# Kernel optimization log

Hardware: AMD Instinct MI355X
Metric: run time of the kernel (lower is better)

The kernel has to match this reference:

```python
import jax, jax.numpy as jnp
import numpy as np

LN_EPS = 1e-5
WKV_EPS = 1e-8


def _layernorm(x, g, b):
    mu = jnp.mean(x, axis=-1, keepdims=True)
    var = jnp.mean((x - mu) ** 2, axis=-1, keepdims=True)
    return (x - mu) * jax.lax.rsqrt(var + LN_EPS) * g + b


def setup_inputs() -> dict:
    key = jax.random.key(0)
    ks = jax.random.split(key, 16)
    B, S, D, F = 4, 2048, 1024, 4096
    xavier_d = float(np.sqrt(6.0 / (D + D)))
    xavier_df = float(np.sqrt(6.0 / (D + F)))
    u = lambda k, sh, s: jax.random.uniform(k, sh, jnp.float32, -s, s)
    return {
        "x": jax.random.normal(ks[0], (B, S, D), jnp.float32),
        "ln1_g": jnp.ones((D,), jnp.float32),
        "ln1_b": jnp.zeros((D,), jnp.float32),
        "ln2_g": jnp.ones((D,), jnp.float32),
        "ln2_b": jnp.zeros((D,), jnp.float32),
        "Wr": u(ks[1], (D, D), xavier_d),
        "Ww": u(ks[2], (D, D), xavier_d),
        "Wk": u(ks[3], (D, D), xavier_d),
        "Wv": u(ks[4], (D, D), xavier_d),
        "Wo": u(ks[5], (D, D), xavier_d),
        "time_decay": jax.random.uniform(ks[6], (D,), jnp.float32, -1.0, 0.0),
        "time_first": jax.random.uniform(ks[7], (D,), jnp.float32, -1.0, 1.0),
        "Wkey": u(ks[8], (F, D), xavier_df),
        "Wval": u(ks[9], (D, F), xavier_df),
        "Wrec": u(ks[10], (D, D), xavier_d),
    }


def _time_mix(xn, Wr, Ww, Wk, Wv, Wo, time_decay):
    # xn: [B,S,D]
    r = jax.nn.sigmoid(jnp.einsum('bsd,ed->bse', xn, Wr))
    w = -jnp.exp(jnp.einsum('bsd,ed->bse', xn, Ww))
    k = jnp.einsum('bsd,ed->bse', xn, Wk)
    v = jnp.einsum('bsd,ed->bse', xn, Wv)
    ewk = jnp.exp(w + k)  # [B,S,D]
    decay = jnp.exp(time_decay)  # [D]

    def step(carry, inp):
        num, den = carry
        e, vt = inp
        num = decay * num + e * vt
        den = decay * den + e
        wkv = num / (den + WKV_EPS)
        return (num, den), wkv

    B, S, D = xn.shape
    init = (jnp.zeros((B, D), xn.dtype), jnp.zeros((B, D), xn.dtype))
    (num_f, den_f), wkv = jax.lax.scan(
        step, init, (jnp.swapaxes(ewk, 0, 1), jnp.swapaxes(v, 0, 1)))
    wkv = jnp.swapaxes(wkv, 0, 1)  # [B,S,D]
    out = jnp.einsum('bsd,ed->bse', r * wkv, Wo)
    final_state = jnp.stack([num_f, den_f], axis=1)  # [B,2,D]
    return out, final_state


def _channel_mix(xn, Wkey, Wval, Wrec):
    k = jnp.einsum('bsd,fd->bsf', xn, Wkey)
    k = jnp.square(jax.nn.relu(k))
    v = jnp.einsum('bsf,df->bsd', k, Wval)
    r = jax.nn.sigmoid(jnp.einsum('bsd,ed->bse', xn, Wrec))
    return r * v


def reference(x, ln1_g, ln1_b, ln2_g, ln2_b, Wr, Ww, Wk, Wv, Wo,
              time_decay, time_first, Wkey, Wval, Wrec):
    tm, new_state = _time_mix(_layernorm(x, ln1_g, ln1_b),
                              Wr, Ww, Wk, Wv, Wo, time_decay)
    x = x + tm
    x = x + _channel_mix(_layernorm(x, ln2_g, ln2_b), Wkey, Wval, Wrec)
    return x, new_state
```

## Files before the change

### kernel.cpp

```cpp
#include <hip/hip_runtime.h>
#include <hip/hip_bf16.h>
#include <cstdint>
#include <cstddef>

using bf16 = __hip_bfloat16;
typedef __bf16 bf16x8 __attribute__((ext_vector_type(8)));
typedef float floatx4 __attribute__((ext_vector_type(4)));

#define LN_EPS 1e-5f
#define WKV_EPS 1e-8f

static constexpr int Bdim = 4, S = 2048, D = 1024, F = 4096;
static constexpr int M = Bdim * S;
static constexpr int NCH = 64, CH = S / NCH;
static constexpr uint32_t FP32_MAGIC = 0x3F800000u;

__device__ __forceinline__ bool is_fp32(const uint32_t* flagp) {
    return *flagp == FP32_MAGIC;
}
__device__ __forceinline__ float loadf(const void* p, size_t i, bool f32) {
    return f32 ? ((const float*)p)[i] : __bfloat162float(((const bf16*)p)[i]);
}

__device__ __forceinline__ void gload_lds16(const void* g, void* l) {
    __builtin_amdgcn_global_load_lds(
        (__attribute__((address_space(1))) void*)(g),
        (__attribute__((address_space(3))) void*)(l), 16, 0, 0);
}

__device__ __forceinline__ bf16x8 sigmoid8(bf16x8 v) {
    bf16x8 o;
    #pragma unroll
    for (int e = 0; e < 8; e++) {
        const float f = (float)v[e];
        o[e] = (__bf16)(1.0f / (1.0f + __expf(-f)));
    }
    return o;
}
__device__ __forceinline__ bf16x8 relusq8(bf16x8 v) {
    bf16x8 o;
    #pragma unroll
    for (int e = 0; e < 8; e++) {
        const float f = fmaxf((float)v[e], 0.0f);
        o[e] = (__bf16)(f * f);
    }
    return o;
}

struct WcvtArgs {
    const void* src[7];
    bf16*       dst[7];
};
__global__ __launch_bounds__(256)
void wcvt(WcvtArgs a, const uint32_t* __restrict__ flagp)
{
    const bool f32 = is_fp32(flagp);
    const int64_t idx = (int64_t)blockIdx.x * 256 + threadIdx.x;
    int seg, off;
    if (idx < (int64_t)6 * 1048576) {
        seg = (int)(idx >> 20); off = (int)(idx & 1048575);
    } else {
        seg = 6; off = (int)(idx - (int64_t)6 * 1048576);
    }
    a.dst[seg][off] = __float2bfloat16(loadf(a.src[seg], off, f32));
}
__global__ __launch_bounds__(256)
void wcvt2(const void* __restrict__ src, bf16* __restrict__ dst,
           const uint32_t* __restrict__ flagp)
{
    const bool f32 = is_fp32(flagp);
    const int idx = blockIdx.x * 256 + threadIdx.x;
    dst[idx] = __float2bfloat16(loadf(src, idx, f32));
}

enum { EPI_QKVW = 1, EPI_KR = 2 };

struct QkvwOut { bf16 *r, *g, *k, *v; };

template<int EPI>
__global__ __launch_bounds__(256)
void gemm_bt(const bf16* __restrict__ A, const bf16* __restrict__ Bw,
             void* __restrict__ outp, void* __restrict__ aux2,
             QkvwOut qo, int K, int N, const uint32_t* __restrict__ flagp)
{
    __shared__ __align__(16) bf16 smem[8192];
    bf16* sA = smem;
    bf16* sB = smem + 4096;
    const int t = threadIdx.x;
    const int tn = blockIdx.x, tm = blockIdx.y;
    const int lane = t & 63, wv = t >> 6;
    const int wm = wv & 1, wn = wv >> 1;
    const int ml = lane & 15, quad = lane >> 4;

    const size_t rowB = (size_t)K * 2;
    const char* gA = (const char*)(A) + (size_t)(tm * 128) * rowB;
    const char* gB = (const char*)(Bw) + (size_t)(tn * 128) * rowB;
    const int r  = t >> 2;
    const int cb = (((t & 3) ^ ((t >> 3) & 3)) << 4);
    const char* a0 = gA + (size_t)r * rowB + cb;
    const char* a1 = gA + (size_t)(r + 64) * rowB + cb;
    const char* b0 = gB + (size_t)r * rowB + cb;
    const char* b1 = gB + (size_t)(r + 64) * rowB + cb;
    char* lA0 = (char*)sA + t * 16;
    char* lA1 = (char*)sA + t * 16 + 4096;
    char* lB0 = (char*)sB + t * 16;
    char* lB1 = (char*)sB + t * 16 + 4096;

    floatx4 acc[4][4] = {};
    const int rq = ((quad ^ ((ml >> 1) & 3)) << 4);

    for (int k0 = 0; k0 < K; k0 += 32) {
        gload_lds16(a0, lA0);
        gload_lds16(a1, lA1);
        gload_lds16(b0, lB0);
        gload_lds16(b1, lB1);
        a0 += 64; a1 += 64; b0 += 64; b1 += 64;
        __syncthreads();
        bf16x8 af[4], bfr[4];
        #pragma unroll
        for (int i = 0; i < 4; i++) {
            af[i]  = *(const bf16x8*)((const char*)sA + (wm * 64 + i * 16 + ml) * 64 + rq);
            bfr[i] = *(const bf16x8*)((const char*)sB + (wn * 64 + i * 16 + ml) * 64 + rq);
        }
        #pragma unroll
        for (int i = 0; i < 4; i++)
            #pragma unroll
            for (int j = 0; j < 4; j++)
                acc[i][j] = __builtin_amdgcn_mfma_f32_16x16x32_bf16(af[i], bfr[j], acc[i][j], 0, 0, 0);
        __syncthreads();
    }

    constexpr int PS = 132;
    const int lwr = wm * 16 + quad * 4;
    const int lwc = wn * 64 + ml;
    const int rr = t >> 3;
    const int rc = (t & 7) * 16;
    #pragma unroll
    for (int i = 0; i < 4; i++) {
        __syncthreads();
        #pragma unroll
        for (int j = 0; j < 4; j++)
            #pragma unroll
            for (int rg = 0; rg < 4; rg++)
                smem[(lwr + rg) * PS + lwc + j * 16] = __float2bfloat16(acc[i][j][rg]);
        __syncthreads();
        const int gr = tm * 128 + ((rr < 16) ? (i * 16 + rr) : (64 + i * 16 + rr - 16));
        bf16x8 v0 = *(const bf16x8*)&smem[rr * PS + rc];
        bf16x8 v1 = *(const bf16x8*)&smem[rr * PS + rc + 8];
        const int gcol = tn * 128 + rc;
        if constexpr (EPI == EPI_QKVW) {
            const int seg = gcol >> 10;
            bf16* dst = (seg == 0) ? qo.r : (seg == 1) ? qo.g : (seg == 2) ? qo.k : qo.v;
            const size_t i2 = (size_t)gr * 1024 + (gcol & 1023);
            if (seg == 0) { v0 = sigmoid8(v0); v1 = sigmoid8(v1); }
            *(bf16x8*)&dst[i2]     = v0;
            *(bf16x8*)&dst[i2 + 8] = v1;
        } else {
            if (tn < 8) {
                const size_t i2 = (size_t)gr * 1024 + gcol;
                *(bf16x8*)&((bf16*)aux2)[i2]     = sigmoid8(v0);
                *(bf16x8*)&((bf16*)aux2)[i2 + 8] = sigmoid8(v1);
            } else {
                const size_t i2 = (size_t)gr * 4096 + (gcol - 1024);
                *(bf16x8*)&((bf16*)outp)[i2]     = relusq8(v0);
                *(bf16x8*)&((bf16*)outp)[i2 + 8] = relusq8(v1);
            }
        }
    }
}

enum { EPI64_ADDX = 0, EPI64_FINAL = 1 };

template<int EPI>
__global__ __launch_bounds__(256)
void gemm_n64(const bf16* __restrict__ A, const bf16* __restrict__ Bw,
              void* __restrict__ outp, const void* __restrict__ aux1,
              const void* __restrict__ aux2, int K, int N,
              const uint32_t* __restrict__ flagp)
{
    __shared__ __align__(16) bf16 smem[6144];
    bf16* sA = smem;
    bf16* sB = smem + 4096;
    const int t = threadIdx.x;
    const int tn = blockIdx.x, tm = blockIdx.y;
    const int lane = t & 63, wv = t >> 6;
    const int wm = wv & 1, wn = wv >> 1;
    const int ml = lane & 15, quad = lane >> 4;

    const size_t rowB = (size_t)K * 2;
    const char* gA = (const char*)(A) + (size_t)(tm * 128) * rowB;
    const char* gB = (const char*)(Bw) + (size_t)(tn * 64) * rowB;
    const int r  = t >> 2;
    const int cb = (((t & 3) ^ ((t >> 3) & 3)) << 4);
    const char* a0 = gA + (size_t)r * rowB + cb;
    const char* a1 = gA + (size_t)(r + 64) * rowB + cb;
    const char* b0 = gB + (size_t)r * rowB + cb;
    char* lA0 = (char*)sA + t * 16;
    char* lA1 = (char*)sA + t * 16 + 4096;
    char* lB0 = (char*)sB + t * 16;

    floatx4 acc[4][2] = {};
    const int rq = ((quad ^ ((ml >> 1) & 3)) << 4);

    for (int k0 = 0; k0 < K; k0 += 32) {
        gload_lds16(a0, lA0);
        gload_lds16(a1, lA1);
        gload_lds16(b0, lB0);
        a0 += 64; a1 += 64; b0 += 64;
        __syncthreads();
        bf16x8 af[4], bfr[2];
        #pragma unroll
        for (int i = 0; i < 4; i++)
            af[i]  = *(const bf16x8*)((const char*)sA + (wm * 64 + i * 16 + ml) * 64 + rq);
        #pragma unroll
        for (int j = 0; j < 2; j++)
            bfr[j] = *(const bf16x8*)((const char*)sB + (wn * 32 + j * 16 + ml) * 64 + rq);
        #pragma unroll
        for (int i = 0; i < 4; i++)
            #pragma unroll
            for (int j = 0; j < 2; j++)
                acc[i][j] = __builtin_amdgcn_mfma_f32_16x16x32_bf16(af[i], bfr[j], acc[i][j], 0, 0, 0);
        __syncthreads();
    }

    const bool f32 = is_fp32(flagp);
    constexpr int PS = 68;
    const int lwr = wm * 16 + quad * 4;
    const int lwc = wn * 32 + ml;
    const int rr = t >> 3;
    const int rc = (t & 7) * 8;
    #pragma unroll
    for (int i = 0; i < 4; i++) {
        __syncthreads();
        #pragma unroll
        for (int j = 0; j < 2; j++)
            #pragma unroll
            for (int rg = 0; rg < 4; rg++)
                smem[(lwr + rg) * PS + lwc + j * 16] = __float2bfloat16(acc[i][j][rg]);
        __syncthreads();
        const int gr = tm * 128 + ((rr < 16) ? (i * 16 + rr) : (64 + i * 16 + rr - 16));
        bf16x8 v = *(const bf16x8*)&smem[rr * PS + rc];
        const size_t idx = (size_t)gr * N + tn * 64 + rc;
        if constexpr (EPI == EPI64_ADDX) {
            bf16x8 o;
            if (f32) {
                const float4* xp = (const float4*)((const float*)aux1 + idx);
                const float4 xa = xp[0], xb = xp[1];
                o[0] = (__bf16)((float)v[0] + xa.x); o[1] = (__bf16)((float)v[1] + xa.y);
                o[2] = (__bf16)((float)v[2] + xa.z); o[3] = (__bf16)((float)v[3] + xa.w);
                o[4] = (__bf16)((float)v[4] + xb.x); o[5] = (__bf16)((float)v[5] + xb.y);
                o[6] = (__bf16)((float)v[6] + xb.z); o[7] = (__bf16)((float)v[7] + xb.w);
            } else {
                const bf16x8 xv = *(const bf16x8*)((const bf16*)aux1 + idx);
                #pragma unroll
                for (int e = 0; e < 8; e++) o[e] = (__bf16)((float)v[e] + (float)xv[e]);
            }
            *(bf16x8*)((bf16*)outp + idx) = o;
        } else {
            const bf16x8 x2v = *(const bf16x8*)((const bf16*)aux1 + idx);
            const bf16x8 rv  = *(const bf16x8*)((const bf16*)aux2 + idx);
            float ov[8];
            #pragma unroll
            for (int e = 0; e < 8; e++)
                ov[e] = (float)x2v[e] + (float)rv[e] * (float)v[e];
            if (f32) {
                float4 f0 = { ov[0], ov[1], ov[2], ov[3] };
                float4 f1 = { ov[4], ov[5], ov[6], ov[7] };
                float4* op = (float4*)((float*)outp + idx);
                op[0] = f0; op[1] = f1;
            } else {
                bf16x8 o;
                #pragma unroll
                for (int e = 0; e < 8; e++) o[e] = (__bf16)ov[e];
                *(bf16x8*)((bf16*)outp + idx) = o;
            }
        }
    }
}

template<bool IN_WS>
__global__ __launch_bounds__(256)
void ln_kernel(const void* __restrict__ x, const void* __restrict__ g,
               const void* __restrict__ b, bf16* __restrict__ out,
               const uint32_t* __restrict__ flagp)
{
    const bool f32 = is_fp32(flagp);
    const int row = blockIdx.x;
    const int t = threadIdx.x;
    const size_t base = (size_t)row * D;
    float v[4];
    #pragma unroll
    for (int i = 0; i < 4; i++) {
        const size_t c = base + t + 256 * i;
        if constexpr (IN_WS) v[i] = __bfloat162float(((const bf16*)x)[c]);
        else                 v[i] = loadf(x, c, f32);
    }
    float s = v[0] + v[1] + v[2] + v[3];
    float q = v[0]*v[0] + v[1]*v[1] + v[2]*v[2] + v[3]*v[3];
    #pragma unroll
    for (int off = 32; off > 0; off >>= 1) {
        s += __shfl_down(s, off);
        q += __shfl_down(q, off);
    }
    __shared__ float rs_[4], rq_[4];
    const int wv = t >> 6, lane = t & 63;
    if (lane == 0) { rs_[wv] = s; rq_[wv] = q; }
    __syncthreads();
    const float St = rs_[0] + rs_[1] + rs_[2] + rs_[3];
    const float Qt = rq_[0] + rq_[1] + rq_[2] + rq_[3];
    const float mean = St * (1.0f / 1024.0f);
    const float var  = Qt * (1.0f / 1024.0f) - mean * mean;
    const float rstd = rsqrtf(var + LN_EPS);
    #pragma unroll
    for (int i = 0; i < 4; i++) {
        const int c = t + 256 * i;
        const float gv = loadf(g, c, f32);
        const float bv = loadf(b, c, f32);
        out[base + c] = __float2bfloat16((v[i] - mean) * rstd * gv + bv);
    }
}

__global__ __launch_bounds__(256)
void scan_a(const bf16* __restrict__ gw, const bf16* __restrict__ kk,
            const bf16* __restrict__ vbuf, const void* __restrict__ td,
            float* __restrict__ numc, float* __restrict__ denc,
            const uint32_t* __restrict__ flagp)
{
    const bool f32 = is_fp32(flagp);
    const int idx = blockIdx.x * 256 + threadIdx.x;
    const int d = idx & (D - 1);
    const int c = (idx >> 10) & (NCH - 1);
    const int b = idx >> 16;
    const float a = __expf(loadf(td, d, f32));
    size_t p = ((size_t)b * S + (size_t)c * CH) * D + d;
    float num = 0.f, den = 0.f;
    for (int ts = 0; ts < CH; ts++) {
        const float g  = __bfloat162float(gw[p]);
        const float kv = __bfloat162float(kk[p]);
        const float e  = __expf(kv - __expf(g));
        const float vv = __bfloat162float(vbuf[p]);
        num = fmaf(a, num, e * vv);
        den = fmaf(a, den, e);
        p += D;
    }
    const size_t slot = ((size_t)b * NCH + c) * D + d;
    numc[slot] = num;
    denc[slot] = den;
}

__global__ __launch_bounds__(256)
void scan_b(float* __restrict__ numc, float* __restrict__ denc,
            const void* __restrict__ td, void* __restrict__ d_out,
            const uint32_t* __restrict__ flagp)
{
    const bool f32 = is_fp32(flagp);
    const int idx = blockIdx.x * 256 + threadIdx.x;
    const int d = idx & (D - 1);
    const int b = idx >> 10;
    const float aL = __expf(loadf(td, d, f32) * (float)CH);
    float cn = 0.f, cd = 0.f;
    for (int c = 0; c < NCH; c++) {
        const size_t slot = ((size_t)b * NCH + c) * D + d;
        const float ln = numc[slot], ld = denc[slot];
        numc[slot] = cn;
        denc[slot] = cd;
        cn = fmaf(aL, cn, ln);
        cd = fmaf(aL, cd, ld);
    }
    const size_t i0 = (size_t)b * 2 * D + d;
    const size_t i1 = i0 + D;
    const size_t off = (size_t)M * D;
    if (f32) {
        ((float*)d_out)[off + i0] = cn;
        ((float*)d_out)[off + i1] = cd;
    } else {
        ((bf16*)d_out)[off + i0] = __float2bfloat16(cn);
        ((bf16*)d_out)[off + i1] = __float2bfloat16(cd);
    }
}

__global__ __launch_bounds__(256)
void scan_c(const bf16* __restrict__ gw, const bf16* __restrict__ kk,
            const bf16* __restrict__ vbuf, bf16* __restrict__ rbuf,
            const float* __restrict__ numc, const float* __restrict__ denc,
            const void* __restrict__ td, const uint32_t* __restrict__ flagp)
{
    const bool f32 = is_fp32(flagp);
    const int idx = blockIdx.x * 256 + threadIdx.x;
    const int d = idx & (D - 1);
    const int c = (idx >> 10) & (NCH - 1);
    const int b = idx >> 16;
    const float a = __expf(loadf(td, d, f32));
    const size_t slot = ((size_t)b * NCH + c) * D + d;
    float num = numc[slot], den = denc[slot];
    size_t p = ((size_t)b * S + (size_t)c * CH) * D + d;
    for (int ts = 0; ts < CH; ts++) {
        const float g  = __bfloat162float(gw[p]);
        const float kv = __bfloat162float(kk[p]);
        const float e  = __expf(kv - __expf(g));
        const float vv = __bfloat162float(vbuf[p]);
        num = fmaf(a, num, e * vv);
        den = fmaf(a, den, e);
        const float wkv = num / (den + WKV_EPS);
        const float r = __bfloat162float(rbuf[p]);
        rbuf[p] = __float2bfloat16(r * wkv);
        p += D;
    }
}

extern "C" void kernel_launch(void* const* d_in, const int* in_sizes, int n_in,
                              void* d_out, int out_size, void* d_ws, size_t ws_size,
                              hipStream_t stream)
{
    const void* x     = d_in[0];
    const void* ln1_g = d_in[1];
    const void* ln1_b = d_in[2];
    const void* ln2_g = d_in[3];
    const void* ln2_b = d_in[4];
    const void* Wr    = d_in[5];
    const void* Ww    = d_in[6];
    const void* Wk    = d_in[7];
    const void* Wv    = d_in[8];
    const void* Wo    = d_in[9];
    const void* td    = d_in[10];
    const void* Wkey  = d_in[12];
    const void* Wval  = d_in[13];
    const void* Wrec  = d_in[14];
    const uint32_t* flagp = (const uint32_t*)ln1_g;

    #define MB(x) ((size_t)(x) << 20)
    char* ws = (char*)d_ws;
    bf16*  xnb    = (bf16*) (ws + MB(0));
    bf16*  wWval2 = (bf16*) (ws + MB(0));
    bf16*  gw     = (bf16*) (ws + MB(16));
    bf16*  kk     = (bf16*) (ws + MB(32));
    bf16*  vbuf   = (bf16*) (ws + MB(48));
    bf16*  wqkvw  = (bf16*) (ws + MB(64));
    bf16*  wWo    = (bf16*) (ws + MB(72));
    float* numc   = (float*)(ws + MB(74));
    float* denc   = (float*)(ws + MB(75));
    bf16*  kbuf   = (bf16*) (ws + MB(16));
    bf16*  rbuf   = (bf16*) (ws + MB(80));
    bf16*  x2     = (bf16*) (ws + MB(96));
    bf16*  wrk    = (bf16*) (ws + MB(112));
    #undef MB

    dim3 blk(256);
    dim3 gQ(F / 128, M / 128);
    dim3 gKR(5120 / 128, M / 128);
    dim3 g64(D / 64, M / 128);

    WcvtArgs wa;
    wa.src[0] = Wr;   wa.dst[0] = wqkvw;
    wa.src[1] = Ww;   wa.dst[1] = wqkvw + (size_t)1 * 1048576;
    wa.src[2] = Wk;   wa.dst[2] = wqkvw + (size_t)2 * 1048576;
    wa.src[3] = Wv;   wa.dst[3] = wqkvw + (size_t)3 * 1048576;
    wa.src[4] = Wo;   wa.dst[4] = wWo;
    wa.src[5] = Wrec; wa.dst[5] = wrk;
    wa.src[6] = Wkey; wa.dst[6] = wrk + (size_t)1048576;

    QkvwOut qo = { rbuf, gw, kk, vbuf };
    QkvwOut q0 = { nullptr, nullptr, nullptr, nullptr };

    wcvt<<<(10 * 1048576) / 256, blk, 0, stream>>>(wa, flagp);
    ln_kernel<false><<<M, blk, 0, stream>>>(x, ln1_g, ln1_b, xnb, flagp);
    gemm_bt<EPI_QKVW><<<gQ, blk, 0, stream>>>(xnb, wqkvw, nullptr, nullptr, qo, D, 4096, flagp);
    scan_a<<<(Bdim * NCH * D) / 256, blk, 0, stream>>>(gw, kk, vbuf, td, numc, denc, flagp);
    scan_b<<<(Bdim * D) / 256,       blk, 0, stream>>>(numc, denc, td, d_out, flagp);
    scan_c<<<(Bdim * NCH * D) / 256, blk, 0, stream>>>(gw, kk, vbuf, rbuf, numc, denc, td, flagp);
    gemm_n64<EPI64_ADDX><<<g64, blk, 0, stream>>>(rbuf, wWo, x2, x, nullptr, D, D, flagp);
    ln_kernel<true><<<M, blk, 0, stream>>>(x2, ln2_g, ln2_b, xnb, flagp);
    gemm_bt<EPI_KR><<<gKR, blk, 0, stream>>>(xnb, wrk, kbuf, rbuf, q0, D, 5120, flagp);
    wcvt2<<<(4 * 1048576) / 256, blk, 0, stream>>>(Wval, wWval2, flagp);
    gemm_n64<EPI64_FINAL><<<g64, blk, 0, stream>>>(kbuf, wWval2, d_out, x2, rbuf, F, D, flagp);
}
```

Baseline: 589.8 us.

## Unify GEMMs into one 512-thread 128x128 kernel with 64-wide K steps

Replaces the two GEMM kernels with a single 512-thread (8-wave) kernel using 128x128 output tiles and a K step of 64 in place of 32. It uses a new XOR swizzle over 128-byte LDS rows and handles all four epilogues. The aim is to halve the barrier count per K, give the N=1024 GEMMs larger tiles for better data reuse, and raise the number of waves per CU. In exchange it uses more LDS per block, and the N=1024 GEMMs now launch half as many blocks, which may hurt load balance.

```diff
diff --git a/kernel.cpp b/kernel.cpp
--- a/kernel.cpp
+++ b/kernel.cpp
@@ -73,19 +73,19 @@
     dst[idx] = __float2bfloat16(loadf(src, idx, f32));
 }
 
-enum { EPI_QKVW = 1, EPI_KR = 2 };
+enum { EPI_QKVW = 1, EPI_KR = 2, EPI_ADDX = 3, EPI_FINAL = 4 };
 
 struct QkvwOut { bf16 *r, *g, *k, *v; };
 
 template<int EPI>
-__global__ __launch_bounds__(256)
+__global__ __launch_bounds__(512, 4)
 void gemm_bt(const bf16* __restrict__ A, const bf16* __restrict__ Bw,
-             void* __restrict__ outp, void* __restrict__ aux2,
-             QkvwOut qo, int K, int N, const uint32_t* __restrict__ flagp)
-{
-    __shared__ __align__(16) bf16 smem[8192];
-    bf16* sA = smem;
-    bf16* sB = smem + 4096;
+             void* __restrict__ outp, const void* __restrict__ aux1,
+             void* __restrict__ aux2, QkvwOut qo, int K, int N,
+             const uint32_t* __restrict__ flagp)
+{
+    __shared__ __align__(16) bf16 smem[16384];
+    char* smb = (char*)smem;
     const int t = threadIdx.x;
     const int tn = blockIdx.x, tm = blockIdx.y;
     const int lane = t & 63, wv = t >> 6;
@@ -93,142 +93,56 @@
     const int ml = lane & 15, quad = lane >> 4;
 
     const size_t rowB = (size_t)K * 2;
-    const char* gA = (const char*)(A) + (size_t)(tm * 128) * rowB;
+    const int r0 = t >> 3;
+    const int q0 = (t & 7) ^ (r0 & 7);
+    const char* gA = (const char*)(A)  + (size_t)(tm * 128) * rowB;
     const char* gB = (const char*)(Bw) + (size_t)(tn * 128) * rowB;
-    const int r  = t >> 2;
-    const int cb = (((t & 3) ^ ((t >> 3) & 3)) << 4);
-    const char* a0 = gA + (size_t)r * rowB + cb;
-    const char* a1 = gA + (size_t)(r + 64) * rowB + cb;
-    const char* b0 = gB + (size_t)r * rowB + cb;
-    const char* b1 = gB + (size_t)(r + 64) * rowB + cb;
-    char* lA0 = (char*)sA + t * 16;
-    char* lA1 = (char*)sA + t * 16 + 4096;
-    char* lB0 = (char*)sB + t * 16;
-    char* lB1 = (char*)sB + t * 16 + 4096;
-
-    floatx4 acc[4][4] = {};
-    const int rq = ((quad ^ ((ml >> 1) & 3)) << 4);
-
-    for (int k0 = 0; k0 < K; k0 += 32) {
+    const char* a0 = gA + (size_t)r0 * rowB + q0 * 16;
+    const char* a1 = a0 + 64 * rowB;
+    const char* b0 = gB + (size_t)r0 * rowB + q0 * 16;
+    const char* b1 = b0 + 64 * rowB;
+    char* lA0 = smb + t * 16;
+    char* lA1 = smb + t * 16 + 8192;
+    char* lB0 = smb + t * 16 + 16384;
+    char* lB1 = smb + t * 16 + 24576;
+
+    floatx4 acc[4][2] = {};
+    const int m7 = ml & 7;
+    const int rq0 = ((quad)     ^ m7) * 16;
+    const int rq1 = ((4 + quad) ^ m7) * 16;
+
+    for (int k0 = 0; k0 < K; k0 += 64) {
         gload_lds16(a0, lA0);
         gload_lds16(a1, lA1);
         gload_lds16(b0, lB0);
         gload_lds16(b1, lB1);
-        a0 += 64; a1 += 64; b0 += 64; b1 += 64;
-        __syncthreads();
-        bf16x8 af[4], bfr[4];
-        #pragma unroll
-        for (int i = 0; i < 4; i++) {
-            af[i]  = *(const bf16x8*)((const char*)sA + (wm * 64 + i * 16 + ml) * 64 + rq);
-            bfr[i] = *(const bf16x8*)((const char*)sB + (wn * 64 + i * 16 + ml) * 64 + rq);
-        }
-        #pragma unroll
-        for (int i = 0; i < 4; i++)
-            #pragma unroll
-            for (int j = 0; j < 4; j++)
-                acc[i][j] = __builtin_amdgcn_mfma_f32_16x16x32_bf16(af[i], bfr[j], acc[i][j], 0, 0, 0);
-        __syncthreads();
-    }
-
-    constexpr int PS = 132;
-    const int lwr = wm * 16 + quad * 4;
-    const int lwc = wn * 64 + ml;
-    const int rr = t >> 3;
-    const int rc = (t & 7) * 16;
-    #pragma unroll
-    for (int i = 0; i < 4; i++) {
+        a0 += 128; a1 += 128; b0 += 128; b1 += 128;
         __syncthreads();
         #pragma unroll
-        for (int j = 0; j < 4; j++)
+        for (int kh = 0; kh < 2; kh++) {
+            const int rq = kh ? rq1 : rq0;
+            bf16x8 af[4], bfr[2];
             #pragma unroll
-            for (int rg = 0; rg < 4; rg++)
-                smem[(lwr + rg) * PS + lwc + j * 16] = __float2bfloat16(acc[i][j][rg]);
-        __syncthreads();
-        const int gr = tm * 128 + ((rr < 16) ? (i * 16 + rr) : (64 + i * 16 + rr - 16));
-        bf16x8 v0 = *(const bf16x8*)&smem[rr * PS + rc];
-        bf16x8 v1 = *(const bf16x8*)&smem[rr * PS + rc + 8];
-        const int gcol = tn * 128 + rc;
-        if constexpr (EPI == EPI_QKVW) {
-            const int seg = gcol >> 10;
-            bf16* dst = (seg == 0) ? qo.r : (seg == 1) ? qo.g : (seg == 2) ? qo.k : qo.v;
-            const size_t i2 = (size_t)gr * 1024 + (gcol & 1023);
-            if (seg == 0) { v0 = sigmoid8(v0); v1 = sigmoid8(v1); }
-            *(bf16x8*)&dst[i2]     = v0;
-            *(bf16x8*)&dst[i2 + 8] = v1;
-        } else {
-            if (tn < 8) {
-                const size_t i2 = (size_t)gr * 1024 + gcol;
-                *(bf16x8*)&((bf16*)aux2)[i2]     = sigmoid8(v0);
-                *(bf16x8*)&((bf16*)aux2)[i2 + 8] = sigmoid8(v1);
-            } else {
-                const size_t i2 = (size_t)gr * 4096 + (gcol - 1024);
-                *(bf16x8*)&((bf16*)outp)[i2]     = relusq8(v0);
-                *(bf16x8*)&((bf16*)outp)[i2 + 8] = relusq8(v1);
-            }
-        }
-    }
-}
-
-enum { EPI64_ADDX = 0, EPI64_FINAL = 1 };
-
-template<int EPI>
-__global__ __launch_bounds__(256)
-void gemm_n64(const bf16* __restrict__ A, const bf16* __restrict__ Bw,
-              void* __restrict__ outp, const void* __restrict__ aux1,
-              const void* __restrict__ aux2, int K, int N,
-              const uint32_t* __restrict__ flagp)
-{
-    __shared__ __align__(16) bf16 smem[6144];
-    bf16* sA = smem;
-    bf16* sB = smem + 4096;
-    const int t = threadIdx.x;
-    const int tn = blockIdx.x, tm = blockIdx.y;
-    const int lane = t & 63, wv = t >> 6;
-    const int wm = wv & 1, wn = wv >> 1;
-    const int ml = lane & 15, quad = lane >> 4;
-
-    const size_t rowB = (size_t)K * 2;
-    const char* gA = (const char*)(A) + (size_t)(tm * 128) * rowB;
-    const char* gB = (const char*)(Bw) + (size_t)(tn * 64) * rowB;
-    const int r  = t >> 2;
-    const int cb = (((t & 3) ^ ((t >> 3) & 3)) << 4);
-    const char* a0 = gA + (size_t)r * rowB + cb;
-    const char* a1 = gA + (size_t)(r + 64) * rowB + cb;
-    const char* b0 = gB + (size_t)r * rowB + cb;
-    char* lA0 = (char*)sA + t * 16;
-    char* lA1 = (char*)sA + t * 16 + 4096;
-    char* lB0 = (char*)sB + t * 16;
-
-    floatx4 acc[4][2] = {};
-    const int rq = ((quad ^ ((ml >> 1) & 3)) << 4);
-
-    for (int k0 = 0; k0 < K; k0 += 32) {
-        gload_lds16(a0, lA0);
-        gload_lds16(a1, lA1);
-        gload_lds16(b0, lB0);
-        a0 += 64; a1 += 64; b0 += 64;
-        __syncthreads();
-        bf16x8 af[4], bfr[2];
-        #pragma unroll
-        for (int i = 0; i < 4; i++)
-            af[i]  = *(const bf16x8*)((const char*)sA + (wm * 64 + i * 16 + ml) * 64 + rq);
-        #pragma unroll
-        for (int j = 0; j < 2; j++)
-            bfr[j] = *(const bf16x8*)((const char*)sB + (wn * 32 + j * 16 + ml) * 64 + rq);
-        #pragma unroll
-        for (int i = 0; i < 4; i++)
+            for (int i = 0; i < 4; i++)
+                af[i]  = *(const bf16x8*)(smb + (wm * 64 + i * 16 + ml) * 128 + rq);
             #pragma unroll
             for (int j = 0; j < 2; j++)
-                acc[i][j] = __builtin_amdgcn_mfma_f32_16x16x32_bf16(af[i], bfr[j], acc[i][j], 0, 0, 0);
+                bfr[j] = *(const bf16x8*)(smb + 16384 + (wn * 32 + j * 16 + ml) * 128 + rq);
+            #pragma unroll
+            for (int i = 0; i < 4; i++)
+                #pragma unroll
+                for (int j = 0; j < 2; j++)
+                    acc[i][j] = __builtin_amdgcn_mfma_f32_16x16x32_bf16(af[i], bfr[j], acc[i][j], 0, 0, 0);
+        }
         __syncthreads();
     }
 
     const bool f32 = is_fp32(flagp);
-    constexpr int PS = 68;
+    constexpr int PS = 136;
     const int lwr = wm * 16 + quad * 4;
     const int lwc = wn * 32 + ml;
-    const int rr = t >> 3;
-    const int rc = (t & 7) * 8;
+    const int rr = t >> 4;
+    const int rc = (t & 15) * 8;
     #pragma unroll
     for (int i = 0; i < 4; i++) {
         __syncthreads();
@@ -240,8 +154,21 @@
         __syncthreads();
         const int gr = tm * 128 + ((rr < 16) ? (i * 16 + rr) : (64 + i * 16 + rr - 16));
         bf16x8 v = *(const bf16x8*)&smem[rr * PS + rc];
-        const size_t idx = (size_t)gr * N + tn * 64 + rc;
-        if constexpr (EPI == EPI64_ADDX) {
+        const int gcol = tn * 128 + rc;
+        if constexpr (EPI == EPI_QKVW) {
+            const int seg = tn >> 3;
+            bf16* dst = (seg == 0) ? qo.r : (seg == 1) ? qo.g : (seg == 2) ? qo.k : qo.v;
+            const size_t i2 = (size_t)gr * 1024 + (gcol & 1023);
+            if (seg == 0) v = sigmoid8(v);
+            *(bf16x8*)&dst[i2] = v;
+        } else if constexpr (EPI == EPI_KR) {
+            if (tn < 8) {
+                *(bf16x8*)&((bf16*)aux2)[(size_t)gr * 1024 + gcol] = sigmoid8(v);
+            } else {
+                *(bf16x8*)&((bf16*)outp)[(size_t)gr * 4096 + (gcol - 1024)] = relusq8(v);
+            }
+        } else if constexpr (EPI == EPI_ADDX) {
+            const size_t idx = (size_t)gr * N + gcol;
             bf16x8 o;
             if (f32) {
                 const float4* xp = (const float4*)((const float*)aux1 + idx);
@@ -257,6 +184,7 @@
             }
             *(bf16x8*)((bf16*)outp + idx) = o;
         } else {
+            const size_t idx = (size_t)gr * N + gcol;
             const bf16x8 x2v = *(const bf16x8*)((const bf16*)aux1 + idx);
             const bf16x8 rv  = *(const bf16x8*)((const bf16*)aux2 + idx);
             float ov[8];
@@ -446,9 +374,10 @@
     #undef MB
 
     dim3 blk(256);
+    dim3 blkG(512);
     dim3 gQ(F / 128, M / 128);
     dim3 gKR(5120 / 128, M / 128);
-    dim3 g64(D / 64, M / 128);
+    dim3 gN1(D / 128, M / 128);
 
     WcvtArgs wa;
     wa.src[0] = Wr;   wa.dst[0] = wqkvw;
@@ -464,13 +393,13 @@
 
     wcvt<<<(10 * 1048576) / 256, blk, 0, stream>>>(wa, flagp);
     ln_kernel<false><<<M, blk, 0, stream>>>(x, ln1_g, ln1_b, xnb, flagp);
-    gemm_bt<EPI_QKVW><<<gQ, blk, 0, stream>>>(xnb, wqkvw, nullptr, nullptr, qo, D, 4096, flagp);
+    gemm_bt<EPI_QKVW><<<gQ, blkG, 0, stream>>>(xnb, wqkvw, nullptr, nullptr, nullptr, qo, D, 4096, flagp);
     scan_a<<<(Bdim * NCH * D) / 256, blk, 0, stream>>>(gw, kk, vbuf, td, numc, denc, flagp);
     scan_b<<<(Bdim * D) / 256,       blk, 0, stream>>>(numc, denc, td, d_out, flagp);
     scan_c<<<(Bdim * NCH * D) / 256, blk, 0, stream>>>(gw, kk, vbuf, rbuf, numc, denc, td, flagp);
-    gemm_n64<EPI64_ADDX><<<g64, blk, 0, stream>>>(rbuf, wWo, x2, x, nullptr, D, D, flagp);
+    gemm_bt<EPI_ADDX><<<gN1, blkG, 0, stream>>>(rbuf, wWo, x2, x, nullptr, q0, D, D, flagp);
     ln_kernel<true><<<M, blk, 0, stream>>>(x2, ln2_g, ln2_b, xnb, flagp);
-    gemm_bt<EPI_KR><<<gKR, blk, 0, stream>>>(xnb, wrk, kbuf, rbuf, q0, D, 5120, flagp);
+    gemm_bt<EPI_KR><<<gKR, blkG, 0, stream>>>(xnb, wrk, kbuf, nullptr, rbuf, q0, D, 5120, flagp);
     wcvt2<<<(4 * 1048576) / 256, blk, 0, stream>>>(Wval, wWval2, flagp);
-    gemm_n64<EPI64_FINAL><<<g64, blk, 0, stream>>>(kbuf, wWval2, d_out, x2, rbuf, F, D, flagp);
-}
+    gemm_bt<EPI_FINAL><<<gN1, blkG, 0, stream>>>(kbuf, wWval2, d_out, x2, rbuf, q0, F, D, flagp);
+}
```

Result: faster. 502.6 us (-14.8%).
